# Performance work log

Hardware: AMD Instinct MI355X
Metric: run time of the kernel (lower is better)

Reference implementation:

```python
import jax, jax.numpy as jnp
import numpy as np

N = 262144        # total nodes
D = 128           # embedding_dim
K = 512           # codebook size
G = 4096          # number of graphs (segments)
T = 10            # num_tasks


def setup_inputs() -> dict:
    key = jax.random.key(0)
    ks = jax.random.split(key, 7)
    x = jax.random.normal(ks[0], (N, D), dtype=jnp.float32)
    batch = jnp.sort(jax.random.randint(ks[1], (N,), 0, G, dtype=jnp.int32)).astype(jnp.int64)
    codebook = jax.random.normal(ks[2], (K, D), dtype=jnp.float32)
    causal_codebook = jax.random.normal(ks[3], (K, D), dtype=jnp.float32)
    counter_codebook = jax.random.normal(ks[4], (K, D), dtype=jnp.float32)
    fc_w = jax.random.normal(ks[5], (T, D), dtype=jnp.float32) * 0.05
    fc_b = jax.random.normal(ks[6], (T,), dtype=jnp.float32) * 0.05
    return {"x": x, "batch": batch, "codebook": codebook,
            "causal_codebook": causal_codebook, "counter_codebook": counter_codebook,
            "fc_w": fc_w, "fc_b": fc_b}


def _global_mean_pool(feat, batch):
    # segment mean over graph ids, fixed num_segments = G
    sums = jax.ops.segment_sum(feat, batch, num_segments=G)
    counts = jax.ops.segment_sum(jnp.ones((feat.shape[0],), feat.dtype), batch, num_segments=G)
    return sums / jnp.maximum(counts, 1.0)[:, None]


def reference(x, batch, codebook, causal_codebook, counter_codebook, fc_w, fc_b):
    batch = batch.astype(jnp.int32)
    pooled_x = _global_mean_pool(x, batch)                      # [G, D]

    # squared euclidean distances (cdist ** 2), [N, K]
    x2 = jnp.sum(x * x, axis=1, keepdims=True)
    c2 = jnp.sum(causal_codebook * causal_codebook, axis=1)
    d2 = x2 + c2[None, :] - 2.0 * (x @ causal_codebook.T)
    indices = jnp.argmin(d2, axis=1)                            # [N]

    selected_causal = causal_codebook[indices]                  # [N, D]
    selected_counter = counter_codebook[indices]                # [N, D]
    causal_output_nodes = x + selected_causal
    counter_output_nodes = selected_counter
    z_nodes = codebook[indices]                                 # [N, D]

    pooled_causal = _global_mean_pool(causal_output_nodes, batch)  # [G, D]
    pooled_counter = _global_mean_pool(counter_output_nodes, batch)

    causal_pre = pooled_causal @ fc_w.T + fc_b                  # [G, T]
    counter_pre = pooled_counter @ fc_w.T + fc_b
    # y_pre uses detached fc params
    w_d = jax.lax.stop_gradient(fc_w)
    b_d = jax.lax.stop_gradient(fc_b)
    y_pre = pooled_x @ w_d.T + b_d
    return (causal_pre, counter_pre, y_pre, z_nodes, pooled_causal, pooled_x)
```

## Files before the change

kernel.cpp:

```cpp
#include <hip/hip_runtime.h>

#define NN 262144
#define DD 128
#define KK 512
#define GG 4096
#define TT 10

#define GT       40960ull
#define Z_OFF    122880ull
#define PC_OFF   33677312ull
#define PX_OFF   34201600ull

#define MARGIN   2.0e-2f


typedef __attribute__((ext_vector_type(8))) short bf16x8;
typedef __attribute__((ext_vector_type(4))) float f32x4;

static __device__ __forceinline__ unsigned short f2bf(float f) {
    unsigned u = __float_as_uint(f);
    return (unsigned short)((u + 0x7FFFu + ((u >> 16) & 1u)) >> 16);
}
static __device__ __forceinline__ float bf2f(unsigned short h) {
    return __uint_as_float(((unsigned)h) << 16);
}

__global__ __launch_bounds__(256) void prep_c2_kernel(const float* __restrict__ ccb,
                                                      float* __restrict__ c2,
                                                      int* __restrict__ flag_cnt) {
    if (blockIdx.x == 0 && threadIdx.x == 0) *flag_cnt = 0;
    const int wid  = (blockIdx.x * 256 + threadIdx.x) >> 6;
    const int lane = threadIdx.x & 63;
    const float* cr = ccb + (size_t)wid * DD;
    float a = cr[2 * lane], b = cr[2 * lane + 1];
    float s = a * a + b * b;
    #pragma unroll
    for (int off = 1; off < 64; off <<= 1) s += __shfl_xor(s, off, 64);
    if (lane == 0) c2[wid] = s;
}

__global__ __launch_bounds__(256) void prep_bpack_kernel(const float* __restrict__ ccb,
                                                         unsigned short* __restrict__ bp) {
    const int i    = blockIdx.x * 256 + threadIdx.x;
    const int lane = i & 63;
    const int s4   = (i >> 6) & 7;
    const int ct   = i >> 9;
    const int code = ct * 16 + (lane & 15);
    const int dim0 = (s4 & 3) * 32 + (lane >> 4) * 8;
    const float* src = ccb + (size_t)code * DD + dim0;
    unsigned short* dst = bp + (size_t)i * 8;
    const bool lo = (s4 >= 4);
    #pragma unroll
    for (int j = 0; j < 8; ++j) {
        float v = src[j];
        unsigned short h = f2bf(v);
        dst[j] = lo ? f2bf(v - bf2f(h)) : h;
    }
}

__global__ __launch_bounds__(256) void argmin_mfma_kernel(
    const float* __restrict__ x, const unsigned short* __restrict__ bp,
    const float* __restrict__ c2, const float* __restrict__ codebook,
    int* __restrict__ idx_out, float* __restrict__ z_out,
    int* __restrict__ flag_cnt, int* __restrict__ flag_list)
{
    const int tid  = threadIdx.x;
    const int lane = tid & 63;
    const int wv   = tid >> 6;
    const int nodebase = blockIdx.x * 128 + wv * 32;
    const int col = lane & 15;
    const int hi  = lane >> 4;

    __shared__ int s_idx[128];

    bf16x8 ah[2][4], al[2][4];
    #pragma unroll
    for (int t = 0; t < 2; ++t) {
        const float* xr = x + (size_t)(nodebase + t * 16 + col) * DD + hi * 8;
        #pragma unroll
        for (int kk = 0; kk < 4; ++kk) {
            float4 u0 = *(const float4*)(xr + kk * 32);
            float4 u1 = *(const float4*)(xr + kk * 32 + 4);
            float f[8] = {u0.x, u0.y, u0.z, u0.w, u1.x, u1.y, u1.z, u1.w};
            bf16x8 H, L;
            #pragma unroll
            for (int j = 0; j < 8; ++j) {
                unsigned short h = f2bf(f[j]);
                H[j] = (short)h;
                L[j] = (short)f2bf(f[j] - bf2f(h));
            }
            ah[t][kk] = H; al[t][kk] = L;
        }
    }

    float b1s[2][4], b2s[2][4]; int b1i[2][4];
    #pragma unroll
    for (int t = 0; t < 2; ++t)
        #pragma unroll
        for (int r = 0; r < 4; ++r) { b1s[t][r] = 3.4e38f; b2s[t][r] = 3.4e38f; b1i[t][r] = 0; }

    const bf16x8* bpf = (const bf16x8*)bp;

    for (int ct = 0; ct < 32; ++ct) {
        bf16x8 bh[4], bl[4];
        #pragma unroll
        for (int kk = 0; kk < 4; ++kk) {
            bh[kk] = bpf[(ct * 8 + kk) * 64 + lane];
            bl[kk] = bpf[(ct * 8 + 4 + kk) * 64 + lane];
        }
        f32x4 acc0 = {0.f, 0.f, 0.f, 0.f}, acc1 = {0.f, 0.f, 0.f, 0.f};
        #pragma unroll
        for (int kk = 0; kk < 4; ++kk) {
            acc0 = __builtin_amdgcn_mfma_f32_16x16x32_bf16(ah[0][kk], bh[kk], acc0, 0, 0, 0);
            acc1 = __builtin_amdgcn_mfma_f32_16x16x32_bf16(ah[1][kk], bh[kk], acc1, 0, 0, 0);
        }
        #pragma unroll
        for (int kk = 0; kk < 4; ++kk) {
            acc0 = __builtin_amdgcn_mfma_f32_16x16x32_bf16(ah[0][kk], bl[kk], acc0, 0, 0, 0);
            acc1 = __builtin_amdgcn_mfma_f32_16x16x32_bf16(ah[1][kk], bl[kk], acc1, 0, 0, 0);
        }
        #pragma unroll
        for (int kk = 0; kk < 4; ++kk) {
            acc0 = __builtin_amdgcn_mfma_f32_16x16x32_bf16(al[0][kk], bh[kk], acc0, 0, 0, 0);
            acc1 = __builtin_amdgcn_mfma_f32_16x16x32_bf16(al[1][kk], bh[kk], acc1, 0, 0, 0);
        }
        #pragma unroll
        for (int kk = 0; kk < 4; ++kk) {
            acc0 = __builtin_amdgcn_mfma_f32_16x16x32_bf16(al[0][kk], bl[kk], acc0, 0, 0, 0);
            acc1 = __builtin_amdgcn_mfma_f32_16x16x32_bf16(al[1][kk], bl[kk], acc1, 0, 0, 0);
        }
        const float c2v  = c2[ct * 16 + col];
        const int   code = ct * 16 + col;
        #pragma unroll
        for (int r = 0; r < 4; ++r) {
            {   float s = fmaf(-2.f, acc0[r], c2v);
                bool lt = s < b1s[0][r];
                float old1 = b1s[0][r];
                float cand2 = lt ? old1 : s;
                b1s[0][r] = lt ? s : old1;
                b1i[0][r] = lt ? code : b1i[0][r];
                b2s[0][r] = fminf(b2s[0][r], cand2); }
            {   float s = fmaf(-2.f, acc1[r], c2v);
                bool lt = s < b1s[1][r];
                float old1 = b1s[1][r];
                float cand2 = lt ? old1 : s;
                b1s[1][r] = lt ? s : old1;
                b1i[1][r] = lt ? code : b1i[1][r];
                b2s[1][r] = fminf(b2s[1][r], cand2); }
        }
    }

    #pragma unroll
    for (int off = 1; off < 16; off <<= 1) {
        #pragma unroll
        for (int t = 0; t < 2; ++t)
            #pragma unroll
            for (int r = 0; r < 4; ++r) {
                float o1s = __shfl_xor(b1s[t][r], off, 64);
                int   o1i = __shfl_xor(b1i[t][r], off, 64);
                float o2s = __shfl_xor(b2s[t][r], off, 64);
                bool owin = (o1s < b1s[t][r]) || (o1s == b1s[t][r] && o1i < b1i[t][r]);
                float loser = owin ? b1s[t][r] : o1s;
                b2s[t][r] = fminf(fminf(b2s[t][r], o2s), loser);
                b1s[t][r] = owin ? o1s : b1s[t][r];
                b1i[t][r] = owin ? o1i : b1i[t][r];
            }
    }

    if (col == 0) {
        #pragma unroll
        for (int t = 0; t < 2; ++t)
            #pragma unroll
            for (int r = 0; r < 4; ++r) {
                const int node = nodebase + t * 16 + hi * 4 + r;
                const int bi = b1i[t][r];
                idx_out[node] = bi;
                s_idx[wv * 32 + t * 16 + hi * 4 + r] = bi;
                if (b2s[t][r] - b1s[t][r] < MARGIN) {
                    int p = atomicAdd(flag_cnt, 1);
                    flag_list[p] = node;
                }
            }
    }
    __syncthreads();

    const int rsub = lane >> 3, csub = lane & 7;
    for (int it = 0; it < 4; ++it) {
        const int lrow = it * 8 + rsub;
        const int bi = s_idx[wv * 32 + lrow];
        const float4* src = (const float4*)(codebook + (size_t)bi * DD) + csub;
        float4* dst = (float4*)(z_out + (size_t)(nodebase + lrow) * DD) + csub;
        #pragma unroll
        for (int j = 0; j < 4; ++j) dst[j * 8] = src[j * 8];
    }
}

__global__ __launch_bounds__(256) void rescore_kernel(
    const float* __restrict__ x, const float* __restrict__ ccb,
    const float* __restrict__ c2, const float* __restrict__ codebook,
    const int* __restrict__ flag_cnt, const int* __restrict__ flag_list,
    int* __restrict__ idx_out, float* __restrict__ z_out)
{
    const int lane = threadIdx.x & 63;
    const int wid  = (blockIdx.x * 256 + threadIdx.x) >> 6;
    const int nw   = gridDim.x * 4;
    const int total = *flag_cnt;
    for (int i = wid; i < total; i += nw) {
        const int node = flag_list[i];
        const float4* x4 = (const float4*)(x + (size_t)node * DD);
        float x2 = 0.f;
        float4 xv[32];
        #pragma unroll
        for (int j = 0; j < 32; ++j) {
            xv[j] = x4[j];
            x2 += xv[j].x * xv[j].x + xv[j].y * xv[j].y
                + xv[j].z * xv[j].z + xv[j].w * xv[j].w;
        }
        unsigned long long best = ~0ull;
        #pragma unroll 2
        for (int c8 = 0; c8 < 8; ++c8) {
            const int k = c8 * 64 + lane;
            const float4* cr = (const float4*)(ccb + (size_t)k * DD);
            float d0 = 0.f, d1 = 0.f, d2 = 0.f, d3 = 0.f;
            #pragma unroll
            for (int j = 0; j < 32; ++j) {
                float4 c = cr[j];
                d0 = fmaf(xv[j].x, c.x, d0);
                d1 = fmaf(xv[j].y, c.y, d1);
                d2 = fmaf(xv[j].z, c.z, d2);
                d3 = fmaf(xv[j].w, c.w, d3);
            }
            float s = (x2 + c2[k]) - 2.f * ((d0 + d1) + (d2 + d3));
            unsigned u = __float_as_uint(s);
            u = (u & 0x80000000u) ? ~u : (u | 0x80000000u);
            unsigned long long key = ((unsigned long long)u << 32) | (unsigned)k;
            best = key < best ? key : best;
        }
        #pragma unroll
        for (int off = 1; off < 64; off <<= 1) {
            unsigned long long o = __shfl_xor(best, off, 64);
            best = o < best ? o : best;
        }
        const int bi = (int)(best & 511u);
        if (lane == 0) idx_out[node] = bi;
        const float* src = codebook + (size_t)bi * DD;
        float2 v; v.x = src[2 * lane]; v.y = src[2 * lane + 1];
        ((float2*)(z_out + (size_t)node * DD))[lane] = v;
    }
}

__global__ __launch_bounds__(512) void pool_kernel(
    const float* __restrict__ x, const void* __restrict__ batch,
    const int* __restrict__ idx, const float* __restrict__ ccb,
    const float* __restrict__ cnb, const float* __restrict__ fcw,
    const float* __restrict__ fcb, float* __restrict__ out)
{
    const int g = blockIdx.x, tid = threadIdx.x;
    const int rid = tid >> 7, d = tid & 127;

    __shared__ int   s_range[2];
    __shared__ float s_red[3][3][128];
    __shared__ float s_pool[3][128];

    const int* b32 = (const int*)batch;
    const bool mode64 = (b32[NN - 1] == 0);

    if (tid == 0) {
        const long long* b64 = (const long long*)batch;
        int lo = 0, hi = NN;
        while (lo < hi) { int mid = (lo + hi) >> 1;
            int v = mode64 ? (int)b64[mid] : b32[mid];
            if (v < g) lo = mid + 1; else hi = mid; }
        s_range[0] = lo;
        hi = NN;
        while (lo < hi) { int mid = (lo + hi) >> 1;
            int v = mode64 ? (int)b64[mid] : b32[mid];
            if (v <= g) lo = mid + 1; else hi = mid; }
        s_range[1] = lo;
    }
    __syncthreads();
    const int start = s_range[0], end = s_range[1];

    float sx = 0.f, sca = 0.f, sco = 0.f;
    for (int n = start + rid; n < end; n += 4) {
        sx += x[(size_t)n * DD + d];
        int k = idx[n];
        sca += ccb[(size_t)k * DD + d];
        sco += cnb[(size_t)k * DD + d];
    }
    if (rid > 0) { s_red[rid - 1][0][d] = sx; s_red[rid - 1][1][d] = sca; s_red[rid - 1][2][d] = sco; }
    __syncthreads();
    if (rid == 0) {
        #pragma unroll
        for (int q = 0; q < 3; ++q) { sx += s_red[q][0][d]; sca += s_red[q][1][d]; sco += s_red[q][2][d]; }
        float cnt = (float)(end - start);
        float inv = 1.f / fmaxf(cnt, 1.f);
        float px  = sx * inv;
        float pca = px + sca * inv;
        float pco = sco * inv;
        out[PX_OFF + (size_t)g * DD + d] = px;
        out[PC_OFF + (size_t)g * DD + d] = pca;
        s_pool[0][d] = pca; s_pool[1][d] = pco; s_pool[2][d] = px;
    }
    __syncthreads();
    if (tid < 3 * TT) {
        int vec = tid / TT, t = tid % TT;
        float a = fcb[t];
        #pragma unroll 8
        for (int j = 0; j < DD; ++j) a = fmaf(s_pool[vec][j], fcw[t * DD + j], a);
        out[(size_t)vec * GT + (size_t)g * TT + t] = a;
    }
}

extern "C" void kernel_launch(void* const* d_in, const int* in_sizes, int n_in,
                              void* d_out, int out_size, void* d_ws, size_t ws_size,
                              hipStream_t stream) {
    const float* x    = (const float*)d_in[0];
    const void*  batch= d_in[1];
    const float* cb   = (const float*)d_in[2];
    const float* ccb  = (const float*)d_in[3];
    const float* cnb  = (const float*)d_in[4];
    const float* fcw  = (const float*)d_in[5];
    const float* fcb  = (const float*)d_in[6];
    float* out = (float*)d_out;

    float* c2  = (float*)d_ws;
    int*   idx = (int*)((char*)d_ws + 4096);
    unsigned short* bpack = (unsigned short*)(out + PC_OFF);
    int* flag_cnt  = (int*)(out + PC_OFF + 65536);
    int* flag_list = (int*)(out + PC_OFF + 65537);

    prep_c2_kernel  <<<128,  256, 0, stream>>>(ccb, c2, flag_cnt);
    prep_bpack_kernel<<<64,  256, 0, stream>>>(ccb, bpack);
    argmin_mfma_kernel<<<2048, 256, 0, stream>>>(x, bpack, c2, cb, idx, out + Z_OFF,
                                                 flag_cnt, flag_list);
    rescore_kernel  <<<128,  256, 0, stream>>>(x, ccb, c2, cb, flag_cnt, flag_list,
                                               idx, out + Z_OFF);
    pool_kernel     <<<GG,   512, 0, stream>>>(x, batch, idx, ccb, cnb, fcw, fcb, out);
}
```

Baseline: 499.7 us.

## Stage codebook tiles in LDS, drop lo*lo MFMA term, vectorize pooling

The argmin kernel now loads each packed codebook tile once per block into a double-buffered shared-memory area, prefetching the next tile during compute, instead of every wave reading it from global memory. The lo*lo product term is dropped and the three remaining terms use separate accumulators to shorten MFMA dependency chains. The pooling kernel switches to float4 loads with 256 threads over 8 row groups. Dropping lo*lo slightly reduces distance precision and the per-tile barrier adds sync cost.

After: 482.6 us. -3.4%, faster.

```diff
diff --git a/kernel.cpp b/kernel.cpp
--- a/kernel.cpp
+++ b/kernel.cpp
@@ -71,6 +71,7 @@
     const int col = lane & 15;
     const int hi  = lane >> 4;
 
+    __shared__ __align__(16) unsigned short sB[2][4096];
     __shared__ int s_idx[128];
 
     bf16x8 ah[2][4], al[2][4];
@@ -99,48 +100,58 @@
         #pragma unroll
         for (int r = 0; r < 4; ++r) { b1s[t][r] = 3.4e38f; b2s[t][r] = 3.4e38f; b1i[t][r] = 0; }
 
-    const bf16x8* bpf = (const bf16x8*)bp;
-
+    {
+        const float4* g4 = (const float4*)bp;
+        float4 r0 = g4[tid], r1 = g4[256 + tid];
+        float4* l4 = (float4*)sB[0];
+        l4[tid] = r0; l4[256 + tid] = r1;
+    }
+    __syncthreads();
+
+    int cur = 0;
     for (int ct = 0; ct < 32; ++ct) {
+        float4 r0, r1;
+        if (ct < 31) {
+            const float4* g4 = (const float4*)(bp + (size_t)(ct + 1) * 4096);
+            r0 = g4[tid]; r1 = g4[256 + tid];
+        }
+
+        const bf16x8* Bv = (const bf16x8*)sB[cur];
         bf16x8 bh[4], bl[4];
         #pragma unroll
         for (int kk = 0; kk < 4; ++kk) {
-            bh[kk] = bpf[(ct * 8 + kk) * 64 + lane];
-            bl[kk] = bpf[(ct * 8 + 4 + kk) * 64 + lane];
-        }
-        f32x4 acc0 = {0.f, 0.f, 0.f, 0.f}, acc1 = {0.f, 0.f, 0.f, 0.f};
+            bh[kk] = Bv[kk * 64 + lane];
+            bl[kk] = Bv[(4 + kk) * 64 + lane];
+        }
+
+        f32x4 aHH0 = {0.f,0.f,0.f,0.f}, aHH1 = aHH0;
+        f32x4 aHL0 = aHH0, aHL1 = aHH0, aLH0 = aHH0, aLH1 = aHH0;
         #pragma unroll
         for (int kk = 0; kk < 4; ++kk) {
-            acc0 = __builtin_amdgcn_mfma_f32_16x16x32_bf16(ah[0][kk], bh[kk], acc0, 0, 0, 0);
-            acc1 = __builtin_amdgcn_mfma_f32_16x16x32_bf16(ah[1][kk], bh[kk], acc1, 0, 0, 0);
-        }
-        #pragma unroll
-        for (int kk = 0; kk < 4; ++kk) {
-            acc0 = __builtin_amdgcn_mfma_f32_16x16x32_bf16(ah[0][kk], bl[kk], acc0, 0, 0, 0);
-            acc1 = __builtin_amdgcn_mfma_f32_16x16x32_bf16(ah[1][kk], bl[kk], acc1, 0, 0, 0);
-        }
-        #pragma unroll
-        for (int kk = 0; kk < 4; ++kk) {
-            acc0 = __builtin_amdgcn_mfma_f32_16x16x32_bf16(al[0][kk], bh[kk], acc0, 0, 0, 0);
-            acc1 = __builtin_amdgcn_mfma_f32_16x16x32_bf16(al[1][kk], bh[kk], acc1, 0, 0, 0);
-        }
-        #pragma unroll
-        for (int kk = 0; kk < 4; ++kk) {
-            acc0 = __builtin_amdgcn_mfma_f32_16x16x32_bf16(al[0][kk], bl[kk], acc0, 0, 0, 0);
-            acc1 = __builtin_amdgcn_mfma_f32_16x16x32_bf16(al[1][kk], bl[kk], acc1, 0, 0, 0);
-        }
+            aHH0 = __builtin_amdgcn_mfma_f32_16x16x32_bf16(ah[0][kk], bh[kk], aHH0, 0, 0, 0);
+            aHH1 = __builtin_amdgcn_mfma_f32_16x16x32_bf16(ah[1][kk], bh[kk], aHH1, 0, 0, 0);
+            aHL0 = __builtin_amdgcn_mfma_f32_16x16x32_bf16(ah[0][kk], bl[kk], aHL0, 0, 0, 0);
+            aHL1 = __builtin_amdgcn_mfma_f32_16x16x32_bf16(ah[1][kk], bl[kk], aHL1, 0, 0, 0);
+            aLH0 = __builtin_amdgcn_mfma_f32_16x16x32_bf16(al[0][kk], bh[kk], aLH0, 0, 0, 0);
+            aLH1 = __builtin_amdgcn_mfma_f32_16x16x32_bf16(al[1][kk], bh[kk], aLH1, 0, 0, 0);
+        }
+
         const float c2v  = c2[ct * 16 + col];
         const int   code = ct * 16 + col;
         #pragma unroll
         for (int r = 0; r < 4; ++r) {
-            {   float s = fmaf(-2.f, acc0[r], c2v);
+            {   float s = fmaf(-2.f, aLH0[r], c2v);
+                s = fmaf(-2.f, aHL0[r], s);
+                s = fmaf(-2.f, aHH0[r], s);
                 bool lt = s < b1s[0][r];
                 float old1 = b1s[0][r];
                 float cand2 = lt ? old1 : s;
                 b1s[0][r] = lt ? s : old1;
                 b1i[0][r] = lt ? code : b1i[0][r];
                 b2s[0][r] = fminf(b2s[0][r], cand2); }
-            {   float s = fmaf(-2.f, acc1[r], c2v);
+            {   float s = fmaf(-2.f, aLH1[r], c2v);
+                s = fmaf(-2.f, aHL1[r], s);
+                s = fmaf(-2.f, aHH1[r], s);
                 bool lt = s < b1s[1][r];
                 float old1 = b1s[1][r];
                 float cand2 = lt ? old1 : s;
@@ -148,6 +159,13 @@
                 b1i[1][r] = lt ? code : b1i[1][r];
                 b2s[1][r] = fminf(b2s[1][r], cand2); }
         }
+
+        if (ct < 31) {
+            float4* l4 = (float4*)sB[cur ^ 1];
+            l4[tid] = r0; l4[256 + tid] = r1;
+        }
+        __syncthreads();
+        cur ^= 1;
     }
 
     #pragma unroll
@@ -249,18 +267,18 @@
     }
 }
 
-__global__ __launch_bounds__(512) void pool_kernel(
+__global__ __launch_bounds__(256) void pool_kernel(
     const float* __restrict__ x, const void* __restrict__ batch,
     const int* __restrict__ idx, const float* __restrict__ ccb,
     const float* __restrict__ cnb, const float* __restrict__ fcw,
     const float* __restrict__ fcb, float* __restrict__ out)
 {
     const int g = blockIdx.x, tid = threadIdx.x;
-    const int rid = tid >> 7, d = tid & 127;
-
-    __shared__ int   s_range[2];
-    __shared__ float s_red[3][3][128];
-    __shared__ float s_pool[3][128];
+    const int q = tid & 31, rid = tid >> 5;
+
+    __shared__ int s_range[2];
+    __shared__ float4 s_red[7][3][32];
+    __shared__ float4 s_pool4[3][32];
 
     const int* b32 = (const int*)batch;
     const bool mode64 = (b32[NN - 1] == 0);
@@ -281,33 +299,44 @@
     __syncthreads();
     const int start = s_range[0], end = s_range[1];
 
-    float sx = 0.f, sca = 0.f, sco = 0.f;
-    for (int n = start + rid; n < end; n += 4) {
-        sx += x[(size_t)n * DD + d];
-        int k = idx[n];
-        sca += ccb[(size_t)k * DD + d];
-        sco += cnb[(size_t)k * DD + d];
-    }
-    if (rid > 0) { s_red[rid - 1][0][d] = sx; s_red[rid - 1][1][d] = sca; s_red[rid - 1][2][d] = sco; }
+    float4 sx = {0.f,0.f,0.f,0.f}, sca = sx, sco = sx;
+    for (int n = start + rid; n < end; n += 8) {
+        const float4 xv = *(const float4*)(x   + (size_t)n * DD + 4 * q);
+        const int k = idx[n];
+        const float4 ca = *(const float4*)(ccb + (size_t)k * DD + 4 * q);
+        const float4 co = *(const float4*)(cnb + (size_t)k * DD + 4 * q);
+        sx.x += xv.x; sx.y += xv.y; sx.z += xv.z; sx.w += xv.w;
+        sca.x += ca.x; sca.y += ca.y; sca.z += ca.z; sca.w += ca.w;
+        sco.x += co.x; sco.y += co.y; sco.z += co.z; sco.w += co.w;
+    }
+    if (rid > 0) { s_red[rid-1][0][q] = sx; s_red[rid-1][1][q] = sca; s_red[rid-1][2][q] = sco; }
     __syncthreads();
     if (rid == 0) {
         #pragma unroll
-        for (int q = 0; q < 3; ++q) { sx += s_red[q][0][d]; sca += s_red[q][1][d]; sco += s_red[q][2][d]; }
+        for (int p = 0; p < 7; ++p) {
+            float4 a = s_red[p][0][q], b = s_red[p][1][q], c = s_red[p][2][q];
+            sx.x += a.x; sx.y += a.y; sx.z += a.z; sx.w += a.w;
+            sca.x += b.x; sca.y += b.y; sca.z += b.z; sca.w += b.w;
+            sco.x += c.x; sco.y += c.y; sco.z += c.z; sco.w += c.w;
+        }
         float cnt = (float)(end - start);
         float inv = 1.f / fmaxf(cnt, 1.f);
-        float px  = sx * inv;
-        float pca = px + sca * inv;
-        float pco = sco * inv;
-        out[PX_OFF + (size_t)g * DD + d] = px;
-        out[PC_OFF + (size_t)g * DD + d] = pca;
-        s_pool[0][d] = pca; s_pool[1][d] = pco; s_pool[2][d] = px;
+        float4 px, pca, pco;
+        px.x = sx.x*inv; px.y = sx.y*inv; px.z = sx.z*inv; px.w = sx.w*inv;
+        pca.x = px.x + sca.x*inv; pca.y = px.y + sca.y*inv;
+        pca.z = px.z + sca.z*inv; pca.w = px.w + sca.w*inv;
+        pco.x = sco.x*inv; pco.y = sco.y*inv; pco.z = sco.z*inv; pco.w = sco.w*inv;
+        *(float4*)(out + PX_OFF + (size_t)g * DD + 4 * q) = px;
+        *(float4*)(out + PC_OFF + (size_t)g * DD + 4 * q) = pca;
+        s_pool4[0][q] = pca; s_pool4[1][q] = pco; s_pool4[2][q] = px;
     }
     __syncthreads();
     if (tid < 3 * TT) {
         int vec = tid / TT, t = tid % TT;
+        const float* sp = (const float*)&s_pool4[vec][0];
         float a = fcb[t];
         #pragma unroll 8
-        for (int j = 0; j < DD; ++j) a = fmaf(s_pool[vec][j], fcw[t * DD + j], a);
+        for (int j = 0; j < DD; ++j) a = fmaf(sp[j], fcw[t * DD + j], a);
         out[(size_t)vec * GT + (size_t)g * TT + t] = a;
     }
 }
@@ -330,11 +359,11 @@
     int* flag_cnt  = (int*)(out + PC_OFF + 65536);
     int* flag_list = (int*)(out + PC_OFF + 65537);
 
-    prep_c2_kernel  <<<128,  256, 0, stream>>>(ccb, c2, flag_cnt);
-    prep_bpack_kernel<<<64,  256, 0, stream>>>(ccb, bpack);
+    prep_c2_kernel   <<<128,  256, 0, stream>>>(ccb, c2, flag_cnt);
+    prep_bpack_kernel<<<64,   256, 0, stream>>>(ccb, bpack);
     argmin_mfma_kernel<<<2048, 256, 0, stream>>>(x, bpack, c2, cb, idx, out + Z_OFF,
                                                  flag_cnt, flag_list);
-    rescore_kernel  <<<128,  256, 0, stream>>>(x, ccb, c2, cb, flag_cnt, flag_list,
-                                               idx, out + Z_OFF);
-    pool_kernel     <<<GG,   512, 0, stream>>>(x, batch, idx, ccb, cnb, fcw, fcb, out);
-}
+    rescore_kernel   <<<128,  256, 0, stream>>>(x, ccb, c2, cb, flag_cnt, flag_list,
+                                                idx, out + Z_OFF);
+    pool_kernel      <<<GG,   256, 0, stream>>>(x, batch, idx, ccb, cnb, fcw, fcb, out);
+}
```
